# Performance work log

Measured on AMD Instinct MI355X. Metric: run time of the kernel, lower is better.

## Reference

```python
import jax, jax.numpy as jnp
import numpy as np
import math

D_MODEL = 512
DK = D_MODEL // 4      # per-head dim = 128
DH = D_MODEL // 8      # half-head dim = 64
BS, QL, SL = 4, 2048, 2048


def setup_inputs() -> dict:
    key = jax.random.key(0)
    ks = jax.random.split(key, 16)
    h = D_MODEL // 2
    inp = {
        "q": jax.random.normal(ks[0], (2, BS, QL, h), jnp.float32),
        "k": jax.random.normal(ks[1], (2, BS, SL, h), jnp.float32),
        "v": jax.random.normal(ks[2], (2, BS, SL, h), jnp.float32),
        "q_spa_embed": jax.random.normal(ks[3], (BS, 1, DK, DK), jnp.float32) * 0.1,
        "kv_spa_embed": jax.random.normal(ks[4], (BS, SL, DK, DK), jnp.float32) * 0.1,
        "attention_bias": jax.random.normal(ks[5], (BS, SL), jnp.float32),
        "mask": jax.random.randint(ks[6], (BS, SL), 0, 2, jnp.int32),
        # Linear weights stored [in, out] (torch Linear(in,out).weight.T)
        "W_qa": jax.random.normal(ks[7], (h, h // 2), jnp.float32) / math.sqrt(h),
        "W_qb": jax.random.normal(ks[8], (h, h // 2), jnp.float32) / math.sqrt(h),
        "W_ka": jax.random.normal(ks[9], (h, h // 2), jnp.float32) / math.sqrt(h),
        "W_kb": jax.random.normal(ks[10], (h, h // 2), jnp.float32) / math.sqrt(h),
        "W_va": jax.random.normal(ks[11], (h, h // 2), jnp.float32) / math.sqrt(h),
        "W_vb": jax.random.normal(ks[12], (h, h // 2), jnp.float32) / math.sqrt(h),
        "W_oa": jax.random.normal(ks[13], (h, h), jnp.float32) / math.sqrt(h),
        "W_ob": jax.random.normal(ks[14], (h, h), jnp.float32) / math.sqrt(h),
    }
    return inp


def _make_heads(xa, xb):
    # xa, xb: [bs, L, d_model//4] -> [bs, 4, L, dk] with head pattern
    # (a0,b0),(a1,b0),(a0,b1),(a1,b1)
    bs, L, _ = xa.shape
    xa = xa.reshape(bs, L, 2, DH)
    xb = xb.reshape(bs, L, 2, DH)
    xa = jnp.tile(xa, (1, 1, 2, 1))            # [bs,L,4,DH]
    xb = jnp.repeat(xb, 2, axis=2)             # [bs,L,4,DH]
    return jnp.concatenate([xa, xb], axis=-1).transpose(0, 2, 1, 3)  # [bs,4,L,DK]


def reference(q, k, v, q_spa_embed, kv_spa_embed, attention_bias, mask,
              W_qa, W_qb, W_ka, W_kb, W_va, W_vb, W_oa, W_ob):
    bs, ql = q.shape[1], q.shape[2]
    sl = k.shape[2]
    qh = _make_heads(q[0] @ W_qa, q[1] @ W_qb)   # [bs,4,ql,DK]
    kh = _make_heads(k[0] @ W_ka, k[1] @ W_kb)   # [bs,4,sl,DK]
    vh = _make_heads(v[0] @ W_va, v[1] @ W_vb)   # [bs,4,sl,DK]

    # per-token spatial rotation (seq_len == kv_spa_embed.shape[1] branch)
    qh = jnp.einsum('bij,bhqj->bhqi', q_spa_embed[:, 0], qh)
    kh = jnp.einsum('bsij,bhsj->bhsi', kv_spa_embed, kh)

    scores = jnp.einsum('bhqd,bhsd->bhqs', qh, kh) / math.sqrt(D_MODEL // 4)
    scores = scores + mask.astype(scores.dtype)[:, None, None, :] * (-1e9)
    attn = jax.nn.softmax(scores - attention_bias[:, None, None, :], axis=-1)
    # dropout: identity (eval mode)
    out = jnp.einsum('bhqs,bhsd->bhqd', attn, vh)          # [bs,4,ql,DK]

    out = out.reshape(bs, 4, ql, 2, DH)
    oa = out[:, :, :, 0].transpose(0, 2, 1, 3).reshape(bs, ql, -1) @ W_oa
    ob = out[:, :, :, 1].transpose(0, 2, 1, 3).reshape(bs, ql, -1) @ W_ob
    return jnp.stack([oa, ob], axis=0), attn
```

## Files before the change

### kernel.cpp

```cpp
#include <hip/hip_runtime.h>
#include <math.h>

#define QL 2048
#define SL 2048
#define BS 4
#define NH 4
#define FSZ ((size_t)BS * QL * 128)

typedef short bf16x8 __attribute__((ext_vector_type(8)));
typedef float f32x4 __attribute__((ext_vector_type(4)));

__device__ __forceinline__ short to_bf16_rne(float x) {
    unsigned u = __float_as_uint(x);
    unsigned r = u + 0x7fffu + ((u >> 16) & 1u);
    return (short)(r >> 16);
}

__global__ __launch_bounds__(256) void proj_gemm(
    const float* __restrict__ q, const float* __restrict__ k, const float* __restrict__ v,
    const float* __restrict__ Wqa, const float* __restrict__ Wqb,
    const float* __restrict__ Wka, const float* __restrict__ Wkb,
    const float* __restrict__ Wva, const float* __restrict__ Wvb,
    float* __restrict__ ws)
{
    int id = blockIdx.z;
    const float* X; const float* W;
    const size_t HALF = (size_t)BS * QL * 256;
    switch (id) {
      case 0: X = q;        W = Wqa; break;
      case 1: X = q + HALF; W = Wqb; break;
      case 2: X = k;        W = Wka; break;
      case 3: X = k + HALF; W = Wkb; break;
      case 4: X = v;        W = Wva; break;
      default:X = v + HALF; W = Wvb; break;
    }
    float* Y = ws + (size_t)id * FSZ;
    int m0 = blockIdx.x * 64;
    int n0 = blockIdx.y * 64;
    __shared__ float At[64][68];
    __shared__ float Bt[64][68];
    int t = threadIdx.x;
    int tx = t & 15, ty = t >> 4;
    float acc[4][4] = {};
    for (int kc = 0; kc < 256; kc += 64) {
        for (int f = t; f < 1024; f += 256) {
            int row = f >> 4, c4 = (f & 15) * 4;
            *(float4*)&At[row][c4] = *(const float4*)(X + (size_t)(m0 + row) * 256 + kc + c4);
        }
        for (int f = t; f < 1024; f += 256) {
            int row = f >> 4, c4 = (f & 15) * 4;
            *(float4*)&Bt[row][c4] = *(const float4*)(W + (size_t)(kc + row) * 128 + n0 + c4);
        }
        __syncthreads();
        for (int j = 0; j < 64; j += 4) {
            float4 a4[4], b4[4];
            #pragma unroll
            for (int i = 0; i < 4; i++) a4[i] = *(const float4*)&At[ty * 4 + i][j];
            #pragma unroll
            for (int jj = 0; jj < 4; jj++) b4[jj] = *(const float4*)&Bt[j + jj][tx * 4];
            #pragma unroll
            for (int i = 0; i < 4; i++) {
                #pragma unroll
                for (int jj = 0; jj < 4; jj++) {
                    float av = ((const float*)&a4[i])[jj];
                    acc[i][0] += av * b4[jj].x;
                    acc[i][1] += av * b4[jj].y;
                    acc[i][2] += av * b4[jj].z;
                    acc[i][3] += av * b4[jj].w;
                }
            }
        }
        __syncthreads();
    }
    for (int i = 0; i < 4; i++) {
        float4 o = make_float4(acc[i][0], acc[i][1], acc[i][2], acc[i][3]);
        *(float4*)(Y + (size_t)(m0 + ty * 4 + i) * 128 + n0 + tx * 4) = o;
    }
}

__global__ __launch_bounds__(256) void rot_split_kernel(
    const float* __restrict__ ha, const float* __restrict__ hb,
    const float* __restrict__ E0, int per_token,
    short* __restrict__ rotS)
{
    int tkn = blockIdx.x;
    int b = blockIdx.y;
    const float* E = E0 + (per_token ? ((size_t)(b * SL + tkn) * 16384)
                                     : ((size_t)b * 16384));
    __shared__ float hv[4][128];
    __shared__ float outl[4][128];
    int tid = threadIdx.x;
    size_t tok = (size_t)(b * QL + tkn) * 128;
    for (int idx = tid; idx < 512; idx += 256) {
        int h = idx >> 7, d = idx & 127;
        float val = (d < 64) ? ha[tok + (h & 1) * 64 + d]
                             : hb[tok + (h >> 1) * 64 + (d - 64)];
        hv[h][d] = val;
    }
    __syncthreads();
    int w = tid >> 6, lane = tid & 63;
    int half = lane >> 5, l5 = lane & 31;
    for (int it = 0; it < 16; ++it) {
        int i = w * 32 + it * 2 + half;
        float4 e = *(const float4*)(E + (size_t)i * 128 + l5 * 4);
        float acc[4];
        #pragma unroll
        for (int h = 0; h < 4; h++) {
            float4 x = *(const float4*)&hv[h][l5 * 4];
            acc[h] = e.x * x.x + e.y * x.y + e.z * x.z + e.w * x.w;
        }
        #pragma unroll
        for (int off = 1; off < 32; off <<= 1) {
            #pragma unroll
            for (int h = 0; h < 4; h++) acc[h] += __shfl_xor(acc[h], off);
        }
        if (l5 < 4) outl[l5][i] = acc[l5];
    }
    __syncthreads();
    if (tid < 128) {
        int h    = tid >> 5;
        int kcid = (tid >> 3) & 3;
        int s    = tid & 7;
        int shalf = s >> 2;
        int isLo  = s & 1;
        int jbase = ((s >> 1) & 1) * 8;
        int dbase = kcid * 32 + shalf * 16 + jbase;
        bf16x8 outv;
        #pragma unroll
        for (int j = 0; j < 8; j++) {
            float x = outl[h][dbase + j];
            short hh = to_bf16_rne(x);
            if (isLo) {
                float hf = __uint_as_float(((unsigned)(unsigned short)hh) << 16);
                outv[j] = to_bf16_rne(x - hf);
            } else {
                outv[j] = hh;
            }
        }
        int bh = b * NH + h;
        int row = tkn & 127;
        size_t base = ((((size_t)bh * 16 + (tkn >> 7)) * 4 + kcid) * 128 + row) * 64;
        *(bf16x8*)&rotS[base + (size_t)((s ^ (row & 7)) * 8)] = outv;
    }
}

__global__ __launch_bounds__(256) void score_mfma_kernel(
    const short* __restrict__ qrotS, const short* __restrict__ krotS,
    const float* __restrict__ bias, const int* __restrict__ mask,
    float* __restrict__ attn, float* __restrict__ stats)
{
    __shared__ short lA[128 * 64];
    __shared__ short lB[128 * 64];
    __shared__ float redM[128][2];
    __shared__ float redS[128][2];

    int bid = blockIdx.x;
    int wg = (bid & 7) * 512 + (bid >> 3);
    int bh = wg >> 8;
    int qt = (wg >> 4) & 15, st = wg & 15;
    int q0 = qt * 128, s0 = st * 128;
    int b = bh >> 2;

    int t = threadIdx.x;
    int l = t & 63, w = t >> 6;
    int wr = w >> 1, wc = w & 1;
    int lr = l & 15, kb = l >> 4;

    const short* Abase = qrotS + (((size_t)bh * 16 + qt) * 4) * 8192;
    const short* Bbase = krotS + (((size_t)bh * 16 + st) * 4) * 8192;

    f32x4 acc[4][4] = {};

    for (int kcid = 0; kcid < 4; kcid++) {
        {
            const bf16x8* srcA = (const bf16x8*)(Abase + (size_t)kcid * 8192) + t * 4;
            const bf16x8* srcB = (const bf16x8*)(Bbase + (size_t)kcid * 8192) + t * 4;
            bf16x8 a0 = srcA[0], a1 = srcA[1], a2 = srcA[2], a3 = srcA[3];
            bf16x8 b0 = srcB[0], b1 = srcB[1], b2 = srcB[2], b3 = srcB[3];
            bf16x8* dA = (bf16x8*)lA + t * 4;
            bf16x8* dB = (bf16x8*)lB + t * 4;
            dA[0] = a0; dA[1] = a1; dA[2] = a2; dA[3] = a3;
            dB[0] = b0; dB[1] = b1; dB[2] = b2; dB[3] = b3;
        }
        __syncthreads();

        bf16x8 ah[4], al[4], bhv[4], blv[4];
        #pragma unroll
        for (int m = 0; m < 4; m++) {
            int r = wr * 64 + m * 16 + lr;
            int r7 = r & 7, base = r * 64;
            ah[m] = *(bf16x8*)&lA[base + (((2 * kb + 0) ^ r7) * 8)];
            al[m] = *(bf16x8*)&lA[base + (((2 * kb + 1) ^ r7) * 8)];
        }
        #pragma unroll
        for (int n = 0; n < 4; n++) {
            int r = wc * 64 + n * 16 + lr;
            int r7 = r & 7, base = r * 64;
            bhv[n] = *(bf16x8*)&lB[base + (((2 * kb + 0) ^ r7) * 8)];
            blv[n] = *(bf16x8*)&lB[base + (((2 * kb + 1) ^ r7) * 8)];
        }
        #pragma unroll
        for (int m = 0; m < 4; m++) {
            #pragma unroll
            for (int n = 0; n < 4; n++) {
                acc[m][n] = __builtin_amdgcn_mfma_f32_16x16x32_bf16(ah[m], bhv[n], acc[m][n], 0, 0, 0);
                acc[m][n] = __builtin_amdgcn_mfma_f32_16x16x32_bf16(ah[m], blv[n], acc[m][n], 0, 0, 0);
                acc[m][n] = __builtin_amdgcn_mfma_f32_16x16x32_bf16(al[m], bhv[n], acc[m][n], 0, 0, 0);
            }
        }
        __syncthreads();
    }

    const float scale = 0.08838834764831845f;
    #pragma unroll
    for (int n = 0; n < 4; n++) {
        int gs = s0 + wc * 64 + n * 16 + lr;
        float adj = -1e9f * (float)mask[b * SL + gs] - bias[b * SL + gs];
        #pragma unroll
        for (int m = 0; m < 4; m++) {
            int gq = q0 + wr * 64 + m * 16 + kb * 4;
            float* dst = attn + ((size_t)bh * QL + gq) * SL + gs;
            f32x4 c = acc[m][n];
            c[0] = c[0] * scale + adj;
            c[1] = c[1] * scale + adj;
            c[2] = c[2] * scale + adj;
            c[3] = c[3] * scale + adj;
            acc[m][n] = c;
            dst[0 * SL] = c[0];
            dst[1 * SL] = c[1];
            dst[2 * SL] = c[2];
            dst[3 * SL] = c[3];
        }
    }

    #pragma unroll
    for (int m = 0; m < 4; m++) {
        #pragma unroll
        for (int i = 0; i < 4; i++) {
            float rm = fmaxf(fmaxf(acc[m][0][i], acc[m][1][i]),
                             fmaxf(acc[m][2][i], acc[m][3][i]));
            rm = fmaxf(rm, __shfl_xor(rm, 1));
            rm = fmaxf(rm, __shfl_xor(rm, 2));
            rm = fmaxf(rm, __shfl_xor(rm, 4));
            rm = fmaxf(rm, __shfl_xor(rm, 8));
            if (lr == 0) redM[wr * 64 + m * 16 + kb * 4 + i][wc] = rm;
        }
    }
    __syncthreads();
    #pragma unroll
    for (int m = 0; m < 4; m++) {
        #pragma unroll
        for (int i = 0; i < 4; i++) {
            int row = wr * 64 + m * 16 + kb * 4 + i;
            float mt = fmaxf(redM[row][0], redM[row][1]);
            float es = __expf(acc[m][0][i] - mt) + __expf(acc[m][1][i] - mt)
                     + __expf(acc[m][2][i] - mt) + __expf(acc[m][3][i] - mt);
            es += __shfl_xor(es, 1);
            es += __shfl_xor(es, 2);
            es += __shfl_xor(es, 4);
            es += __shfl_xor(es, 8);
            if (lr == 0) redS[row][wc] = es;
        }
    }
    __syncthreads();
    if (t < 128) {
        float mt = fmaxf(redM[t][0], redM[t][1]);
        float es = redS[t][0] + redS[t][1];
        size_t r = (size_t)bh * QL + q0 + t;
        stats[(r * 16 + st) * 2 + 0] = mt;
        stats[(r * 16 + st) * 2 + 1] = es;
    }
}

__global__ __launch_bounds__(256) void sreduce_kernel(
    const float* __restrict__ stats,
    float* __restrict__ rowm, float* __restrict__ rowinv)
{
    int r = blockIdx.x * 256 + threadIdx.x;
    const float* src = stats + (size_t)r * 32;
    float4 p[8];
    #pragma unroll
    for (int j = 0; j < 8; j++) p[j] = *(const float4*)(src + j * 4);
    float m = -INFINITY;
    #pragma unroll
    for (int j = 0; j < 8; j++) { m = fmaxf(m, p[j].x); m = fmaxf(m, p[j].z); }
    float s = 0.f;
    #pragma unroll
    for (int j = 0; j < 8; j++) {
        s += p[j].y * __expf(p[j].x - m);
        s += p[j].w * __expf(p[j].z - m);
    }
    rowm[r] = m;
    rowinv[r] = 1.0f / s;
}

__global__ __launch_bounds__(256) void vtrans_kernel(
    const float* __restrict__ va, const float* __restrict__ vb,
    short* __restrict__ vT)
{
    int sblk = blockIdx.x;
    int bh = blockIdx.y;
    int b = bh >> 2, h = bh & 3;
    int hao = (h & 1) * 64, hbo = (h >> 1) * 64;
    __shared__ float vt[32][132];
    int t = threadIdx.x;
    for (int f = t; f < 1024; f += 256) {
        int s = f >> 5, c4 = (f & 31) * 4;
        size_t tok = (size_t)(b * SL + sblk * 32 + s) * 128;
        float4 vv = (c4 < 64) ? *(const float4*)(va + tok + hao + c4)
                              : *(const float4*)(vb + tok + hbo + (c4 - 64));
        *(float4*)&vt[s][c4] = vv;
    }
    __syncthreads();
    int d = t >> 1, shalf = t & 1;
    bf16x8 hi[2], lo[2];
    #pragma unroll
    for (int kb2 = 0; kb2 < 2; kb2++) {
        int kb = shalf * 2 + kb2;
        #pragma unroll
        for (int j = 0; j < 8; j++) {
            float x = vt[kb * 8 + j][d];
            short hh = to_bf16_rne(x);
            float hf = __uint_as_float(((unsigned)(unsigned short)hh) << 16);
            hi[kb2][j] = hh;
            lo[kb2][j] = to_bf16_rne(x - hf);
        }
    }
    size_t base = (((size_t)bh * 64 + sblk) * 128 + d) * 64;
    int d7 = d & 7;
    *(bf16x8*)&vT[base + (size_t)(((2 * (shalf * 2 + 0) + 0) ^ d7) * 8)] = hi[0];
    *(bf16x8*)&vT[base + (size_t)(((2 * (shalf * 2 + 0) + 1) ^ d7) * 8)] = lo[0];
    *(bf16x8*)&vT[base + (size_t)(((2 * (shalf * 2 + 1) + 0) ^ d7) * 8)] = hi[1];
    *(bf16x8*)&vT[base + (size_t)(((2 * (shalf * 2 + 1) + 1) ^ d7) * 8)] = lo[1];
}

__global__ __launch_bounds__(256) void pv_fused_kernel(
    float* __restrict__ attn, const short* __restrict__ vT,
    const float* __restrict__ rowm, const float* __restrict__ rowinv,
    float* __restrict__ outh)
{
    __shared__ short lA[128 * 64];
    __shared__ short lB[128 * 64];

    int bid = blockIdx.x;
    int wg = (bid & 7) * 32 + (bid >> 3);
    int bh = wg >> 4, qt = wg & 15;
    int q0 = qt * 128;

    float* Ag = attn + ((size_t)bh * QL + q0) * SL;
    const short* Bg = vT + (size_t)bh * 64 * 8192;

    int t = threadIdx.x;
    int srow = t >> 1, shalf = t & 1;
    int l = t & 63, w = t >> 6;
    int wr = w >> 1, wc = w & 1;
    int lr = l & 15, kb = l >> 4;

    float rm  = rowm[(size_t)bh * QL + q0 + srow];
    float riv = rowinv[(size_t)bh * QL + q0 + srow];

    f32x4 acc[4][4] = {};

    for (int sblk = 0; sblk < 64; sblk++) {
        {
            float* src = Ag + (size_t)srow * SL + sblk * 32 + shalf * 16;
            float x[16];
            #pragma unroll
            for (int j = 0; j < 4; j++)
                *(float4*)&x[j * 4] = *(const float4*)(src + j * 4);
            #pragma unroll
            for (int j = 0; j < 16; j++)
                x[j] = __expf(x[j] - rm) * riv;
            #pragma unroll
            for (int j = 0; j < 4; j++)
                *(float4*)(src + j * 4) = *(float4*)&x[j * 4];
            bf16x8 h0, l0, h1, l1;
            #pragma unroll
            for (int j = 0; j < 8; j++) {
                short hh = to_bf16_rne(x[j]);
                float hf = __uint_as_float(((unsigned)(unsigned short)hh) << 16);
                h0[j] = hh; l0[j] = to_bf16_rne(x[j] - hf);
                hh = to_bf16_rne(x[j + 8]);
                hf = __uint_as_float(((unsigned)(unsigned short)hh) << 16);
                h1[j] = hh; l1[j] = to_bf16_rne(x[j + 8] - hf);
            }
            int base = srow * 64, r7 = srow & 7;
            *(bf16x8*)&lA[base + (((4 * shalf + 0) ^ r7) * 8)] = h0;
            *(bf16x8*)&lA[base + (((4 * shalf + 1) ^ r7) * 8)] = l0;
            *(bf16x8*)&lA[base + (((4 * shalf + 2) ^ r7) * 8)] = h1;
            *(bf16x8*)&lA[base + (((4 * shalf + 3) ^ r7) * 8)] = l1;
        }
        {
            const bf16x8* src = (const bf16x8*)(Bg + (size_t)sblk * 8192) + t * 4;
            bf16x8 v0 = src[0], v1 = src[1], v2 = src[2], v3 = src[3];
            bf16x8* dst = (bf16x8*)lB + t * 4;
            dst[0] = v0; dst[1] = v1; dst[2] = v2; dst[3] = v3;
        }
        __syncthreads();

        bf16x8 ah[4], al[4], bhv[4], blv[4];
        #pragma unroll
        for (int m = 0; m < 4; m++) {
            int r = wr * 64 + m * 16 + lr;
            int r7 = r & 7, base = r * 64;
            ah[m] = *(bf16x8*)&lA[base + (((2 * kb + 0) ^ r7) * 8)];
            al[m] = *(bf16x8*)&lA[base + (((2 * kb + 1) ^ r7) * 8)];
        }
        #pragma unroll
        for (int n = 0; n < 4; n++) {
            int r = wc * 64 + n * 16 + lr;
            int r7 = r & 7, base = r * 64;
            bhv[n] = *(bf16x8*)&lB[base + (((2 * kb + 0) ^ r7) * 8)];
            blv[n] = *(bf16x8*)&lB[base + (((2 * kb + 1) ^ r7) * 8)];
        }
        #pragma unroll
        for (int m = 0; m < 4; m++) {
            #pragma unroll
            for (int n = 0; n < 4; n++) {
                acc[m][n] = __builtin_amdgcn_mfma_f32_16x16x32_bf16(ah[m], bhv[n], acc[m][n], 0, 0, 0);
                acc[m][n] = __builtin_amdgcn_mfma_f32_16x16x32_bf16(ah[m], blv[n], acc[m][n], 0, 0, 0);
                acc[m][n] = __builtin_amdgcn_mfma_f32_16x16x32_bf16(al[m], bhv[n], acc[m][n], 0, 0, 0);
            }
        }
        __syncthreads();
    }

    #pragma unroll
    for (int n = 0; n < 4; n++) {
        int gd = wc * 64 + n * 16 + lr;
        #pragma unroll
        for (int m = 0; m < 4; m++) {
            int gq = q0 + wr * 64 + m * 16 + kb * 4;
            float* dst = outh + ((size_t)bh * QL + gq) * 128 + gd;
            f32x4 c = acc[m][n];
            dst[0 * 128] = c[0];
            dst[1 * 128] = c[1];
            dst[2 * 128] = c[2];
            dst[3 * 128] = c[3];
        }
    }
}

__global__ __launch_bounds__(256) void oproj_kernel(
    const float* __restrict__ outh, const float* __restrict__ Woa, const float* __restrict__ Wob,
    float* __restrict__ outp)
{
    int bid = blockIdx.x;
    int sel = bid >> 9;
    int rem = bid & 511;
    int b = rem >> 7;
    int rem2 = rem & 127;
    int tt = rem2 >> 2, ot = rem2 & 3;
    int t0 = tt * 64, o0 = ot * 64;
    const float* W = sel ? Wob : Woa;
    int doff = sel ? 64 : 0;
    __shared__ float At[64][68];
    __shared__ float Bt[64][68];
    int t = threadIdx.x;
    int tx = t & 15, ty = t >> 4;
    float acc[4][4] = {};
    for (int kc = 0; kc < 256; kc += 64) {
        int h = kc >> 6;
        for (int f = t; f < 1024; f += 256) {
            int row = f >> 4, c4 = (f & 15) * 4;
            *(float4*)&At[row][c4] =
                *(const float4*)(outh + ((size_t)(b * NH + h) * QL + t0 + row) * 128 + doff + c4);
        }
        for (int f = t; f < 1024; f += 256) {
            int row = f >> 4, c4 = (f & 15) * 4;
            *(float4*)&Bt[row][c4] = *(const float4*)(W + (size_t)(kc + row) * 256 + o0 + c4);
        }
        __syncthreads();
        for (int j = 0; j < 64; j += 4) {
            float4 a4[4], b4[4];
            #pragma unroll
            for (int i = 0; i < 4; i++) a4[i] = *(const float4*)&At[ty * 4 + i][j];
            #pragma unroll
            for (int jj = 0; jj < 4; jj++) b4[jj] = *(const float4*)&Bt[j + jj][tx * 4];
            #pragma unroll
            for (int i = 0; i < 4; i++) {
                #pragma unroll
                for (int jj = 0; jj < 4; jj++) {
                    float av = ((const float*)&a4[i])[jj];
                    acc[i][0] += av * b4[jj].x;
                    acc[i][1] += av * b4[jj].y;
                    acc[i][2] += av * b4[jj].z;
                    acc[i][3] += av * b4[jj].w;
                }
            }
        }
        __syncthreads();
    }
    for (int i = 0; i < 4; i++) {
        float4 o = make_float4(acc[i][0], acc[i][1], acc[i][2], acc[i][3]);
        *(float4*)(outp + ((size_t)((sel * BS + b) * QL) + t0 + ty * 4 + i) * 256 + o0 + tx * 4) = o;
    }
}

extern "C" void kernel_launch(void* const* d_in, const int* in_sizes, int n_in,
                              void* d_out, int out_size, void* d_ws, size_t ws_size,
                              hipStream_t stream)
{
    const float* q    = (const float*)d_in[0];
    const float* k    = (const float*)d_in[1];
    const float* v    = (const float*)d_in[2];
    const float* qse  = (const float*)d_in[3];
    const float* kvse = (const float*)d_in[4];
    const float* bias = (const float*)d_in[5];
    const int*   mask = (const int*)d_in[6];
    const float* Wqa  = (const float*)d_in[7];
    const float* Wqb  = (const float*)d_in[8];
    const float* Wka  = (const float*)d_in[9];
    const float* Wkb  = (const float*)d_in[10];
    const float* Wva  = (const float*)d_in[11];
    const float* Wvb  = (const float*)d_in[12];
    const float* Woa  = (const float*)d_in[13];
    const float* Wob  = (const float*)d_in[14];

    float* outp = (float*)d_out;
    float* attn = outp + (size_t)2 * BS * QL * 256;

    float* ws     = (float*)d_ws;
    float* qa     = ws + 0 * FSZ;
    float* qb     = ws + 1 * FSZ;
    float* ka     = ws + 2 * FSZ;
    float* kb     = ws + 3 * FSZ;
    float* va     = ws + 4 * FSZ;
    float* vb     = ws + 5 * FSZ;
    short* qrotS  = (short*)(ws + 6 * FSZ);
    short* krotS  = (short*)(ws + 10 * FSZ);
    float* outh   = ws + 14 * FSZ;
    float* stats  = outh;
    short* vT     = (short*)(ws + 18 * FSZ);
    float* rowm   = ws + 22 * FSZ;
    float* rowinv = ws + 22 * FSZ + 32768;

    proj_gemm<<<dim3(128, 2, 6), 256, 0, stream>>>(q, k, v, Wqa, Wqb, Wka, Wkb, Wva, Wvb, ws);
    vtrans_kernel<<<dim3(64, 16), 256, 0, stream>>>(va, vb, vT);
    rot_split_kernel<<<dim3(QL, BS), 256, 0, stream>>>(qa, qb, qse, 0, qrotS);
    rot_split_kernel<<<dim3(SL, BS), 256, 0, stream>>>(ka, kb, kvse, 1, krotS);
    score_mfma_kernel<<<4096, 256, 0, stream>>>(qrotS, krotS, bias, mask, attn, stats);
    sreduce_kernel<<<128, 256, 0, stream>>>(stats, rowm, rowinv);
    pv_fused_kernel<<<256, 256, 0, stream>>>(attn, vT, rowm, rowinv, outh);
    oproj_kernel<<<1024, 256, 0, stream>>>(outh, Woa, Wob, outp);
}
```

Measured before the change: 658.7 us.

## Split PV kernel over key dimension into four partial sums reduced in oproj

```diff
diff --git a/kernel.cpp b/kernel.cpp
--- a/kernel.cpp
+++ b/kernel.cpp
@@ -337,18 +337,20 @@
 __global__ __launch_bounds__(256) void pv_fused_kernel(
     float* __restrict__ attn, const short* __restrict__ vT,
     const float* __restrict__ rowm, const float* __restrict__ rowinv,
-    float* __restrict__ outh)
+    float* __restrict__ outh_part)
 {
     __shared__ short lA[128 * 64];
     __shared__ short lB[128 * 64];
 
     int bid = blockIdx.x;
-    int wg = (bid & 7) * 32 + (bid >> 3);
-    int bh = wg >> 4, qt = wg & 15;
+    int wg = (bid & 7) * 128 + (bid >> 3);
+    int ks = wg >> 8;
+    int bh = (wg >> 4) & 15, qt = wg & 15;
     int q0 = qt * 128;
 
     float* Ag = attn + ((size_t)bh * QL + q0) * SL;
     const short* Bg = vT + (size_t)bh * 64 * 8192;
+    float* Og = outh_part + (size_t)ks * 4 * FSZ;
 
     int t = threadIdx.x;
     int srow = t >> 1, shalf = t & 1;
@@ -361,7 +363,7 @@
 
     f32x4 acc[4][4] = {};
 
-    for (int sblk = 0; sblk < 64; sblk++) {
+    for (int sblk = ks * 16; sblk < ks * 16 + 16; sblk++) {
         {
             float* src = Ag + (size_t)srow * SL + sblk * 32 + shalf * 16;
             float x[16];
@@ -431,7 +433,7 @@
         #pragma unroll
         for (int m = 0; m < 4; m++) {
             int gq = q0 + wr * 64 + m * 16 + kb * 4;
-            float* dst = outh + ((size_t)bh * QL + gq) * 128 + gd;
+            float* dst = Og + ((size_t)bh * QL + gq) * 128 + gd;
             f32x4 c = acc[m][n];
             dst[0 * 128] = c[0];
             dst[1 * 128] = c[1];
@@ -442,7 +444,7 @@
 }
 
 __global__ __launch_bounds__(256) void oproj_kernel(
-    const float* __restrict__ outh, const float* __restrict__ Woa, const float* __restrict__ Wob,
+    const float* __restrict__ outh_part, const float* __restrict__ Woa, const float* __restrict__ Wob,
     float* __restrict__ outp)
 {
     int bid = blockIdx.x;
@@ -459,12 +461,21 @@
     int t = threadIdx.x;
     int tx = t & 15, ty = t >> 4;
     float acc[4][4] = {};
+    const size_t PSTRIDE = (size_t)4 * FSZ;
     for (int kc = 0; kc < 256; kc += 64) {
         int h = kc >> 6;
         for (int f = t; f < 1024; f += 256) {
             int row = f >> 4, c4 = (f & 15) * 4;
-            *(float4*)&At[row][c4] =
-                *(const float4*)(outh + ((size_t)(b * NH + h) * QL + t0 + row) * 128 + doff + c4);
+            size_t off = ((size_t)(b * NH + h) * QL + t0 + row) * 128 + doff + c4;
+            float4 s0 = *(const float4*)(outh_part + off);
+            float4 s1 = *(const float4*)(outh_part + PSTRIDE + off);
+            float4 s2 = *(const float4*)(outh_part + 2 * PSTRIDE + off);
+            float4 s3 = *(const float4*)(outh_part + 3 * PSTRIDE + off);
+            float4 sum = make_float4(s0.x + s1.x + s2.x + s3.x,
+                                     s0.y + s1.y + s2.y + s3.y,
+                                     s0.z + s1.z + s2.z + s3.z,
+                                     s0.w + s1.w + s2.w + s3.w);
+            *(float4*)&At[row][c4] = sum;
         }
         for (int f = t; f < 1024; f += 256) {
             int row = f >> 4, c4 = (f & 15) * 4;
@@ -529,11 +540,11 @@
     float* vb     = ws + 5 * FSZ;
     short* qrotS  = (short*)(ws + 6 * FSZ);
     short* krotS  = (short*)(ws + 10 * FSZ);
-    float* outh   = ws + 14 * FSZ;
-    float* stats  = outh;
-    short* vT     = (short*)(ws + 18 * FSZ);
-    float* rowm   = ws + 22 * FSZ;
-    float* rowinv = ws + 22 * FSZ + 32768;
+    float* stats  = ws + 14 * FSZ;
+    float* rowm   = ws + 15 * FSZ;
+    float* rowinv = ws + 15 * FSZ + 32768;
+    short* vT     = (short*)(ws + 16 * FSZ);
+    float* ohp    = ws + 20 * FSZ;
 
     proj_gemm<<<dim3(128, 2, 6), 256, 0, stream>>>(q, k, v, Wqa, Wqb, Wka, Wkb, Wva, Wvb, ws);
     vtrans_kernel<<<dim3(64, 16), 256, 0, stream>>>(va, vb, vT);
@@ -541,6 +552,6 @@
     rot_split_kernel<<<dim3(SL, BS), 256, 0, stream>>>(ka, kb, kvse, 1, krotS);
     score_mfma_kernel<<<4096, 256, 0, stream>>>(qrotS, krotS, bias, mask, attn, stats);
     sreduce_kernel<<<128, 256, 0, stream>>>(stats, rowm, rowinv);
-    pv_fused_kernel<<<256, 256, 0, stream>>>(attn, vT, rowm, rowinv, outh);
-    oproj_kernel<<<1024, 256, 0, stream>>>(outh, Woa, Wob, outp);
-}
+    pv_fused_kernel<<<1024, 256, 0, stream>>>(attn, vT, rowm, rowinv, ohp);
+    oproj_kernel<<<1024, 256, 0, stream>>>(ohp, Woa, Wob, outp);
+}
```

Measured after the change: 679.5 us. 1.03x slower.

## Port input and output projection GEMMs to split-bf16 MFMA kernels

Applied to the files above, without the earlier changes.

```diff
diff --git a/kernel.cpp b/kernel.cpp
--- a/kernel.cpp
+++ b/kernel.cpp
@@ -16,14 +16,24 @@
     return (short)(r >> 16);
 }
 
-__global__ __launch_bounds__(256) void proj_gemm(
+__device__ __forceinline__ void split8(const float* x, bf16x8& hi, bf16x8& lo) {
+    #pragma unroll
+    for (int j = 0; j < 8; j++) {
+        short hh = to_bf16_rne(x[j]);
+        float hf = __uint_as_float(((unsigned)(unsigned short)hh) << 16);
+        hi[j] = hh;
+        lo[j] = to_bf16_rne(x[j] - hf);
+    }
+}
+
+__global__ __launch_bounds__(256) void proj_mfma_kernel(
     const float* __restrict__ q, const float* __restrict__ k, const float* __restrict__ v,
     const float* __restrict__ Wqa, const float* __restrict__ Wqb,
     const float* __restrict__ Wka, const float* __restrict__ Wkb,
     const float* __restrict__ Wva, const float* __restrict__ Wvb,
     float* __restrict__ ws)
 {
-    int id = blockIdx.z;
+    int id = blockIdx.y;
     const float* X; const float* W;
     const size_t HALF = (size_t)BS * QL * 256;
     switch (id) {
@@ -35,46 +45,92 @@
       default:X = v + HALF; W = Wvb; break;
     }
     float* Y = ws + (size_t)id * FSZ;
-    int m0 = blockIdx.x * 64;
-    int n0 = blockIdx.y * 64;
-    __shared__ float At[64][68];
-    __shared__ float Bt[64][68];
+    int m0 = blockIdx.x * 128;
+
+    __shared__ short lA[128 * 64];
+    __shared__ short lB[128 * 64];
+
     int t = threadIdx.x;
-    int tx = t & 15, ty = t >> 4;
-    float acc[4][4] = {};
-    for (int kc = 0; kc < 256; kc += 64) {
-        for (int f = t; f < 1024; f += 256) {
-            int row = f >> 4, c4 = (f & 15) * 4;
-            *(float4*)&At[row][c4] = *(const float4*)(X + (size_t)(m0 + row) * 256 + kc + c4);
-        }
-        for (int f = t; f < 1024; f += 256) {
-            int row = f >> 4, c4 = (f & 15) * 4;
-            *(float4*)&Bt[row][c4] = *(const float4*)(W + (size_t)(kc + row) * 128 + n0 + c4);
-        }
-        __syncthreads();
-        for (int j = 0; j < 64; j += 4) {
-            float4 a4[4], b4[4];
-            #pragma unroll
-            for (int i = 0; i < 4; i++) a4[i] = *(const float4*)&At[ty * 4 + i][j];
-            #pragma unroll
-            for (int jj = 0; jj < 4; jj++) b4[jj] = *(const float4*)&Bt[j + jj][tx * 4];
-            #pragma unroll
-            for (int i = 0; i < 4; i++) {
-                #pragma unroll
-                for (int jj = 0; jj < 4; jj++) {
-                    float av = ((const float*)&a4[i])[jj];
-                    acc[i][0] += av * b4[jj].x;
-                    acc[i][1] += av * b4[jj].y;
-                    acc[i][2] += av * b4[jj].z;
-                    acc[i][3] += av * b4[jj].w;
-                }
+    int srow = t >> 1, shalf = t & 1;
+    int l = t & 63, w = t >> 6;
+    int wr = w >> 1, wc = w & 1;
+    int lr = l & 15, kb = l >> 4;
+
+    f32x4 acc[4][4] = {};
+
+    for (int kc = 0; kc < 256; kc += 32) {
+        {
+            const float* srcA = X + (size_t)(m0 + srow) * 256 + kc + shalf * 16;
+            float xa[16];
+            #pragma unroll
+            for (int j = 0; j < 4; j++)
+                *(float4*)&xa[j * 4] = *(const float4*)(srcA + j * 4);
+            bf16x8 h0, l0, h1, l1;
+            split8(&xa[0], h0, l0);
+            split8(&xa[8], h1, l1);
+            int base = srow * 64, r7 = srow & 7;
+            *(bf16x8*)&lA[base + (((4 * shalf + 0) ^ r7) * 8)] = h0;
+            *(bf16x8*)&lA[base + (((4 * shalf + 1) ^ r7) * 8)] = l0;
+            *(bf16x8*)&lA[base + (((4 * shalf + 2) ^ r7) * 8)] = h1;
+            *(bf16x8*)&lA[base + (((4 * shalf + 3) ^ r7) * 8)] = l1;
+        }
+        {
+            int ncol = srow;
+            float xb[16];
+            #pragma unroll
+            for (int j = 0; j < 16; j++)
+                xb[j] = W[(size_t)(kc + shalf * 16 + j) * 128 + ncol];
+            bf16x8 h0, l0, h1, l1;
+            split8(&xb[0], h0, l0);
+            split8(&xb[8], h1, l1);
+            int base = ncol * 64, r7 = ncol & 7;
+            *(bf16x8*)&lB[base + (((4 * shalf + 0) ^ r7) * 8)] = h0;
+            *(bf16x8*)&lB[base + (((4 * shalf + 1) ^ r7) * 8)] = l0;
+            *(bf16x8*)&lB[base + (((4 * shalf + 2) ^ r7) * 8)] = h1;
+            *(bf16x8*)&lB[base + (((4 * shalf + 3) ^ r7) * 8)] = l1;
+        }
+        __syncthreads();
+
+        bf16x8 ah[4], al[4], bhv[4], blv[4];
+        #pragma unroll
+        for (int m = 0; m < 4; m++) {
+            int r = wr * 64 + m * 16 + lr;
+            int r7 = r & 7, base = r * 64;
+            ah[m] = *(bf16x8*)&lA[base + (((2 * kb + 0) ^ r7) * 8)];
+            al[m] = *(bf16x8*)&lA[base + (((2 * kb + 1) ^ r7) * 8)];
+        }
+        #pragma unroll
+        for (int n = 0; n < 4; n++) {
+            int r = wc * 64 + n * 16 + lr;
+            int r7 = r & 7, base = r * 64;
+            bhv[n] = *(bf16x8*)&lB[base + (((2 * kb + 0) ^ r7) * 8)];
+            blv[n] = *(bf16x8*)&lB[base + (((2 * kb + 1) ^ r7) * 8)];
+        }
+        #pragma unroll
+        for (int m = 0; m < 4; m++) {
+            #pragma unroll
+            for (int n = 0; n < 4; n++) {
+                acc[m][n] = __builtin_amdgcn_mfma_f32_16x16x32_bf16(ah[m], bhv[n], acc[m][n], 0, 0, 0);
+                acc[m][n] = __builtin_amdgcn_mfma_f32_16x16x32_bf16(ah[m], blv[n], acc[m][n], 0, 0, 0);
+                acc[m][n] = __builtin_amdgcn_mfma_f32_16x16x32_bf16(al[m], bhv[n], acc[m][n], 0, 0, 0);
             }
         }
         __syncthreads();
     }
-    for (int i = 0; i < 4; i++) {
-        float4 o = make_float4(acc[i][0], acc[i][1], acc[i][2], acc[i][3]);
-        *(float4*)(Y + (size_t)(m0 + ty * 4 + i) * 128 + n0 + tx * 4) = o;
+
+    #pragma unroll
+    for (int n = 0; n < 4; n++) {
+        int gcol = wc * 64 + n * 16 + lr;
+        #pragma unroll
+        for (int m = 0; m < 4; m++) {
+            int grow = m0 + wr * 64 + m * 16 + kb * 4;
+            float* dst = Y + (size_t)grow * 128 + gcol;
+            f32x4 c = acc[m][n];
+            dst[0 * 128] = c[0];
+            dst[1 * 128] = c[1];
+            dst[2 * 128] = c[2];
+            dst[3 * 128] = c[3];
+        }
     }
 }
 
@@ -375,15 +431,8 @@
             for (int j = 0; j < 4; j++)
                 *(float4*)(src + j * 4) = *(float4*)&x[j * 4];
             bf16x8 h0, l0, h1, l1;
-            #pragma unroll
-            for (int j = 0; j < 8; j++) {
-                short hh = to_bf16_rne(x[j]);
-                float hf = __uint_as_float(((unsigned)(unsigned short)hh) << 16);
-                h0[j] = hh; l0[j] = to_bf16_rne(x[j] - hf);
-                hh = to_bf16_rne(x[j + 8]);
-                hf = __uint_as_float(((unsigned)(unsigned short)hh) << 16);
-                h1[j] = hh; l1[j] = to_bf16_rne(x[j + 8] - hf);
-            }
+            split8(&x[0], h0, l0);
+            split8(&x[8], h1, l1);
             int base = srow * 64, r7 = srow & 7;
             *(bf16x8*)&lA[base + (((4 * shalf + 0) ^ r7) * 8)] = h0;
             *(bf16x8*)&lA[base + (((4 * shalf + 1) ^ r7) * 8)] = l0;
@@ -441,59 +490,104 @@
     }
 }
 
-__global__ __launch_bounds__(256) void oproj_kernel(
+__global__ __launch_bounds__(256) void oproj_mfma_kernel(
     const float* __restrict__ outh, const float* __restrict__ Woa, const float* __restrict__ Wob,
     float* __restrict__ outp)
 {
-    int bid = blockIdx.x;
-    int sel = bid >> 9;
-    int rem = bid & 511;
-    int b = rem >> 7;
-    int rem2 = rem & 127;
-    int tt = rem2 >> 2, ot = rem2 & 3;
-    int t0 = tt * 64, o0 = ot * 64;
+    int bt = blockIdx.x;
+    int b = bt >> 4, tt = bt & 15;
+    int t0 = tt * 128;
+    int n0 = blockIdx.y * 128;
+    int sel = blockIdx.z;
     const float* W = sel ? Wob : Woa;
     int doff = sel ? 64 : 0;
-    __shared__ float At[64][68];
-    __shared__ float Bt[64][68];
+
+    __shared__ short lA[128 * 64];
+    __shared__ short lB[128 * 64];
+
     int t = threadIdx.x;
-    int tx = t & 15, ty = t >> 4;
-    float acc[4][4] = {};
-    for (int kc = 0; kc < 256; kc += 64) {
-        int h = kc >> 6;
-        for (int f = t; f < 1024; f += 256) {
-            int row = f >> 4, c4 = (f & 15) * 4;
-            *(float4*)&At[row][c4] =
-                *(const float4*)(outh + ((size_t)(b * NH + h) * QL + t0 + row) * 128 + doff + c4);
-        }
-        for (int f = t; f < 1024; f += 256) {
-            int row = f >> 4, c4 = (f & 15) * 4;
-            *(float4*)&Bt[row][c4] = *(const float4*)(W + (size_t)(kc + row) * 256 + o0 + c4);
-        }
-        __syncthreads();
-        for (int j = 0; j < 64; j += 4) {
-            float4 a4[4], b4[4];
-            #pragma unroll
-            for (int i = 0; i < 4; i++) a4[i] = *(const float4*)&At[ty * 4 + i][j];
-            #pragma unroll
-            for (int jj = 0; jj < 4; jj++) b4[jj] = *(const float4*)&Bt[j + jj][tx * 4];
-            #pragma unroll
-            for (int i = 0; i < 4; i++) {
-                #pragma unroll
-                for (int jj = 0; jj < 4; jj++) {
-                    float av = ((const float*)&a4[i])[jj];
-                    acc[i][0] += av * b4[jj].x;
-                    acc[i][1] += av * b4[jj].y;
-                    acc[i][2] += av * b4[jj].z;
-                    acc[i][3] += av * b4[jj].w;
-                }
+    int srow = t >> 1, shalf = t & 1;
+    int l = t & 63, w = t >> 6;
+    int wr = w >> 1, wc = w & 1;
+    int lr = l & 15, kb = l >> 4;
+
+    f32x4 acc[4][4] = {};
+
+    for (int kc = 0; kc < 256; kc += 32) {
+        {
+            int k0 = kc + shalf * 16;
+            int h = k0 >> 6, d0 = k0 & 63;
+            const float* srcA = outh + ((size_t)(b * NH + h) * QL + t0 + srow) * 128 + doff + d0;
+            float xa[16];
+            #pragma unroll
+            for (int j = 0; j < 4; j++)
+                *(float4*)&xa[j * 4] = *(const float4*)(srcA + j * 4);
+            bf16x8 h0, l0, h1, l1;
+            split8(&xa[0], h0, l0);
+            split8(&xa[8], h1, l1);
+            int base = srow * 64, r7 = srow & 7;
+            *(bf16x8*)&lA[base + (((4 * shalf + 0) ^ r7) * 8)] = h0;
+            *(bf16x8*)&lA[base + (((4 * shalf + 1) ^ r7) * 8)] = l0;
+            *(bf16x8*)&lA[base + (((4 * shalf + 2) ^ r7) * 8)] = h1;
+            *(bf16x8*)&lA[base + (((4 * shalf + 3) ^ r7) * 8)] = l1;
+        }
+        {
+            int ncol = srow;
+            float xb[16];
+            #pragma unroll
+            for (int j = 0; j < 16; j++)
+                xb[j] = W[(size_t)(kc + shalf * 16 + j) * 256 + n0 + ncol];
+            bf16x8 h0, l0, h1, l1;
+            split8(&xb[0], h0, l0);
+            split8(&xb[8], h1, l1);
+            int base = ncol * 64, r7 = ncol & 7;
+            *(bf16x8*)&lB[base + (((4 * shalf + 0) ^ r7) * 8)] = h0;
+            *(bf16x8*)&lB[base + (((4 * shalf + 1) ^ r7) * 8)] = l0;
+            *(bf16x8*)&lB[base + (((4 * shalf + 2) ^ r7) * 8)] = h1;
+            *(bf16x8*)&lB[base + (((4 * shalf + 3) ^ r7) * 8)] = l1;
+        }
+        __syncthreads();
+
+        bf16x8 ah[4], al[4], bhv[4], blv[4];
+        #pragma unroll
+        for (int m = 0; m < 4; m++) {
+            int r = wr * 64 + m * 16 + lr;
+            int r7 = r & 7, base = r * 64;
+            ah[m] = *(bf16x8*)&lA[base + (((2 * kb + 0) ^ r7) * 8)];
+            al[m] = *(bf16x8*)&lA[base + (((2 * kb + 1) ^ r7) * 8)];
+        }
+        #pragma unroll
+        for (int n = 0; n < 4; n++) {
+            int r = wc * 64 + n * 16 + lr;
+            int r7 = r & 7, base = r * 64;
+            bhv[n] = *(bf16x8*)&lB[base + (((2 * kb + 0) ^ r7) * 8)];
+            blv[n] = *(bf16x8*)&lB[base + (((2 * kb + 1) ^ r7) * 8)];
+        }
+        #pragma unroll
+        for (int m = 0; m < 4; m++) {
+            #pragma unroll
+            for (int n = 0; n < 4; n++) {
+                acc[m][n] = __builtin_amdgcn_mfma_f32_16x16x32_bf16(ah[m], bhv[n], acc[m][n], 0, 0, 0);
+                acc[m][n] = __builtin_amdgcn_mfma_f32_16x16x32_bf16(ah[m], blv[n], acc[m][n], 0, 0, 0);
+                acc[m][n] = __builtin_amdgcn_mfma_f32_16x16x32_bf16(al[m], bhv[n], acc[m][n], 0, 0, 0);
             }
         }
         __syncthreads();
     }
-    for (int i = 0; i < 4; i++) {
-        float4 o = make_float4(acc[i][0], acc[i][1], acc[i][2], acc[i][3]);
-        *(float4*)(outp + ((size_t)((sel * BS + b) * QL) + t0 + ty * 4 + i) * 256 + o0 + tx * 4) = o;
+
+    #pragma unroll
+    for (int n = 0; n < 4; n++) {
+        int gcol = n0 + wc * 64 + n * 16 + lr;
+        #pragma unroll
+        for (int m = 0; m < 4; m++) {
+            int grow = t0 + wr * 64 + m * 16 + kb * 4;
+            float* dst = outp + ((size_t)((sel * BS + b) * QL) + grow) * 256 + gcol;
+            f32x4 c = acc[m][n];
+            dst[0 * 256] = c[0];
+            dst[1 * 256] = c[1];
+            dst[2 * 256] = c[2];
+            dst[3 * 256] = c[3];
+        }
     }
 }
 
@@ -529,18 +623,18 @@
     float* vb     = ws + 5 * FSZ;
     short* qrotS  = (short*)(ws + 6 * FSZ);
     short* krotS  = (short*)(ws + 10 * FSZ);
-    float* outh   = ws + 14 * FSZ;
-    float* stats  = outh;
-    short* vT     = (short*)(ws + 18 * FSZ);
-    float* rowm   = ws + 22 * FSZ;
-    float* rowinv = ws + 22 * FSZ + 32768;
-
-    proj_gemm<<<dim3(128, 2, 6), 256, 0, stream>>>(q, k, v, Wqa, Wqb, Wka, Wkb, Wva, Wvb, ws);
+    float* stats  = ws + 14 * FSZ;
+    float* rowm   = ws + 15 * FSZ;
+    float* rowinv = ws + 15 * FSZ + 32768;
+    short* vT     = (short*)(ws + 16 * FSZ);
+    float* outh   = ws + 20 * FSZ;
+
+    proj_mfma_kernel<<<dim3(64, 6), 256, 0, stream>>>(q, k, v, Wqa, Wqb, Wka, Wkb, Wva, Wvb, ws);
     vtrans_kernel<<<dim3(64, 16), 256, 0, stream>>>(va, vb, vT);
     rot_split_kernel<<<dim3(QL, BS), 256, 0, stream>>>(qa, qb, qse, 0, qrotS);
     rot_split_kernel<<<dim3(SL, BS), 256, 0, stream>>>(ka, kb, kvse, 1, krotS);
     score_mfma_kernel<<<4096, 256, 0, stream>>>(qrotS, krotS, bias, mask, attn, stats);
     sreduce_kernel<<<128, 256, 0, stream>>>(stats, rowm, rowinv);
     pv_fused_kernel<<<256, 256, 0, stream>>>(attn, vT, rowm, rowinv, outh);
-    oproj_kernel<<<1024, 256, 0, stream>>>(outh, Woa, Wob, outp);
-}
+    oproj_mfma_kernel<<<dim3(64, 2, 2), 256, 0, stream>>>(outh, Woa, Wob, outp);
+}
```

After: 623.1 us. 5.4% less time.
